# Performance work log

Measured on AMD Instinct MI355X. Metric: run time of the kernel, lower is better.

## Reference

```python
import jax, jax.numpy as jnp
import numpy as np

B, S, D = 1, 2048, 4096
N_HEADS, N_KV_HEADS = 32, 8
HEAD_DIM = D // N_HEADS  # 128


def setup_inputs() -> dict:
    key = jax.random.key(0)
    ks = jax.random.split(key, 6)
    x = jax.random.normal(ks[0], (B, S, D), dtype=jnp.float32)
    # weights stored as [in, out] so forward is x @ W (== torch x @ W.T with W [out,in])
    sc = 0.02
    wq = jax.random.normal(ks[1], (D, N_HEADS * HEAD_DIM), dtype=jnp.float32) * sc
    wk = jax.random.normal(ks[2], (D, N_KV_HEADS * HEAD_DIM), dtype=jnp.float32) * sc
    wv = jax.random.normal(ks[3], (D, N_KV_HEADS * HEAD_DIM), dtype=jnp.float32) * sc
    wo = jax.random.normal(ks[4], (N_HEADS * HEAD_DIM, D), dtype=jnp.float32) * sc
    # rotary tables: freqs_cis as cos/sin of shape [S, HEAD_DIM//2]
    inv_freq = 1.0 / (10000.0 ** (np.arange(0, HEAD_DIM, 2, dtype=np.float32) / HEAD_DIM))
    t = np.arange(S, dtype=np.float32)
    freqs = np.outer(t, inv_freq)  # [S, HEAD_DIM//2]
    cos = jnp.asarray(np.cos(freqs), dtype=jnp.float32)
    sin = jnp.asarray(np.sin(freqs), dtype=jnp.float32)
    # additive causal mask [S, S]: 0 on/below diagonal, -inf above
    mask = jnp.where(jnp.tril(jnp.ones((S, S), dtype=bool)), 0.0, -1e9).astype(jnp.float32)
    return {"x": x, "wq": wq, "wk": wk, "wv": wv, "wo": wo,
            "cos": cos, "sin": sin, "mask": mask}


def _apply_rope(t, cos, sin):
    # t: [B, S, H, Hd]; interpret last dim as Hd//2 complex pairs (interleaved)
    b, s, h, hd = t.shape
    tr = t.reshape(b, s, h, hd // 2, 2)
    t1, t2 = tr[..., 0], tr[..., 1]
    c = cos[None, :, None, :]  # [1, S, 1, Hd//2]
    sn = sin[None, :, None, :]
    o1 = t1 * c - t2 * sn
    o2 = t1 * sn + t2 * c
    return jnp.stack([o1, o2], axis=-1).reshape(b, s, h, hd)


def reference(x, wq, wk, wv, wo, cos, sin, mask):
    b, s, d = x.shape
    hd = 2 * cos.shape[-1]
    nh = wq.shape[1] // hd
    nkv = wk.shape[1] // hd
    n_rep = nh // nkv
    q = (x @ wq).reshape(b, s, nh, hd)
    k = (x @ wk).reshape(b, s, nkv, hd)
    v = (x @ wv).reshape(b, s, nkv, hd)
    q = _apply_rope(q, cos, sin)
    k = _apply_rope(k, cos, sin)
    # repeat_kv along head dim
    k = jnp.repeat(k, n_rep, axis=2)  # [B, S, H, Hd]
    v = jnp.repeat(v, n_rep, axis=2)
    scale = 1.0 / jnp.sqrt(jnp.float32(hd))
    scores = jnp.einsum('bqhd,bkhd->bhqk', q, k) * scale + mask[None, None, :, :]
    probs = jax.nn.softmax(scores, axis=-1)
    out = jnp.einsum('bhqk,bkhd->bqhd', probs, v).reshape(b, s, nh * hd)
    return out @ wo
```

## Files before the change

kernel.cpp:

```cpp
#include <hip/hip_runtime.h>
#include <hip/hip_bf16.h>

typedef unsigned short u16;
typedef unsigned int   u32;
typedef __attribute__((ext_vector_type(8))) short bf16x8;
typedef __attribute__((ext_vector_type(4))) short bf16x4;
typedef __attribute__((ext_vector_type(4))) float f32x4;
typedef __attribute__((ext_vector_type(4))) unsigned short u16x4;

__device__ __forceinline__ u16 f32_to_bf16bits(float f) {
    u32 x = __float_as_uint(f);
    u32 r = (x + 0x7fffu + ((x >> 16) & 1u)) >> 16;
    return (u16)r;
}
__device__ __forceinline__ float bf16bits_to_f32(u16 u) {
    return __uint_as_float(((u32)u) << 16);
}
__device__ __forceinline__ u32 cvt_pk_bf16(float lo, float hi) {
    u32 r;
    asm("v_cvt_pk_bf16_f32 %0, %1, %2" : "=v"(r) : "v"(lo), "v"(hi));
    return r;
}

__device__ __forceinline__ void async_copy16(void* lds, const void* g) {
    __builtin_amdgcn_global_load_lds(
        (__attribute__((address_space(1))) void*)(g),
        (__attribute__((address_space(3))) void*)(lds), 16, 0, 0);
}

__global__ void convert_f32_bf16(const float* __restrict__ src, u16* __restrict__ dst, int n4) {
    const int i = blockIdx.x * 256 + threadIdx.x;
    if (i >= n4) return;
    const float4 v = ((const float4*)src)[i];
    u16x4 o = { f32_to_bf16bits(v.x), f32_to_bf16bits(v.y),
                f32_to_bf16bits(v.z), f32_to_bf16bits(v.w) };
    ((u16x4*)dst)[i] = o;
}

__global__ void transpose_wT(const float* __restrict__ src, u16* __restrict__ dst,
                             int N, int dstStride) {
    __shared__ float tile[32][129];
    const int n0 = blockIdx.x * 128, k0 = blockIdx.y * 32;
    const int tx = threadIdx.x, ty = threadIdx.y;
#pragma unroll
    for (int j = 0; j < 4; ++j)
#pragma unroll
        for (int i = 0; i < 4; ++i)
            tile[ty + 8*j][tx + 32*i] = src[(size_t)(k0 + ty + 8*j) * N + n0 + tx + 32*i];
    __syncthreads();
    const int tid = ty * 32 + tx;
    const int c = tid & 15, nl0 = tid >> 4;
#pragma unroll
    for (int s = 0; s < 8; ++s) {
        const int nl = nl0 + s * 16;
        const u32 pk = (u32)f32_to_bf16bits(tile[2*c][nl])
                     | ((u32)f32_to_bf16bits(tile[2*c + 1][nl]) << 16);
        *(u32*)&dst[(size_t)(n0 + nl) * dstStride + k0 + 2*c] = pk;
    }
}

__global__ void transpose_v(const u16* __restrict__ qkv, u16* __restrict__ vT) {
    __shared__ u16 tile[32][34];
    const int s0 = blockIdx.x * 32, n0 = blockIdx.y * 32;
    const int tx = threadIdx.x, ty = threadIdx.y;
#pragma unroll
    for (int i = 0; i < 4; ++i)
        tile[ty + i*8][tx] = qkv[(size_t)(s0 + ty + i*8) * 6144 + 5120 + n0 + tx];
    __syncthreads();
#pragma unroll
    for (int i = 0; i < 4; ++i)
        vT[(size_t)(n0 + ty + i*8) * 2048 + s0 + tx] = tile[tx][ty + i*8];
}

__global__ void rope_kernel(u32* __restrict__ qkv, const float* __restrict__ cosp,
                            const float* __restrict__ sinp) {
    const int s = blockIdx.x;
    const int h = blockIdx.y * 4 + (threadIdx.x >> 6);
    const int p = threadIdx.x & 63;
    const size_t off = ((size_t)s * 6144 + h * 128) >> 1;
    const u32 packed = qkv[off + p];
    const float c  = cosp[s*64 + p], sn = sinp[s*64 + p];
    const float t1 = bf16bits_to_f32((u16)(packed & 0xffffu));
    const float t2 = bf16bits_to_f32((u16)(packed >> 16));
    const float o1 = t1 * c - t2 * sn;
    const float o2 = t1 * sn + t2 * c;
    qkv[off + p] = (u32)f32_to_bf16bits(o1) | ((u32)f32_to_bf16bits(o2) << 16);
}

template<int MFRAG, bool BF16OUT>
__global__ __launch_bounds__(512, 2) void gemm_ring(
    const u16* __restrict__ A, const u16* __restrict__ B, void* __restrict__ Cv,
    int N, int K, int nbn) {
    constexpr int BM     = MFRAG * 32;
    constexpr int ABYTES = BM * 64;
    constexpr int SLOT   = ABYTES + 16384;
    __shared__ __align__(16) char sm[4 * SLOT];

    const int tid = threadIdx.x;
    const int w = tid >> 6, l = tid & 63;
    const int wm = w >> 2, wn = w & 3;
    const int g = l >> 4, c0 = l & 15;
    const int bid = blockIdx.x;
    const int bm = bid / nbn, bn = bid % nbn;

    const int srow   = l >> 2;
    const int schunk = (l & 3) ^ (srow & 3) ^ ((srow >> 2) & 3);
    const u16* As = A + (size_t)(bm * BM  + w*16 + srow) * K + schunk * 8;
    const u16* Bs = B + (size_t)(bn * 256 + w*16 + srow) * K + schunk * 8;

    const int rswz = ((g ^ (c0 & 3) ^ ((c0 >> 2) & 3)) & 3) * 16;

    f32x4 acc[MFRAG][4] = {};

    auto stage = [&](int st, int ss) {
        char* aB = sm + ss * SLOT;
        char* bB = aB + ABYTES;
        const u16* as = As + (size_t)st * 32;
        const u16* bs = Bs + (size_t)st * 32;
        async_copy16(aB + (w*16) * 64, as);
        if (MFRAG == 8)
            async_copy16(aB + (128 + w*16) * 64, as + (size_t)128 * K);
        async_copy16(bB + (w*16) * 64, bs);
        async_copy16(bB + (128 + w*16) * 64, bs + (size_t)128 * K);
    };

    const int nkt = K >> 5;
    stage(0, 0);
    stage(1, 1);

    for (int kt = 0; kt < nkt; ++kt) {
        const int st = (kt + 2 < nkt) ? kt + 2 : nkt - 1;
        stage(st, (kt + 2) & 3);
        if (MFRAG == 8) asm volatile("s_waitcnt vmcnt(8)" ::: "memory");
        else            asm volatile("s_waitcnt vmcnt(6)" ::: "memory");
        __builtin_amdgcn_s_barrier();
        asm volatile("" ::: "memory");

        const char* aB = sm + (kt & 3) * SLOT;
        const char* bB = aB + ABYTES;
        bf16x8 bfr[4];
#pragma unroll
        for (int n = 0; n < 4; ++n)
            bfr[n] = *(const bf16x8*)(bB + (wn*64 + n*16 + c0) * 64 + rswz);
        bf16x8 afr[MFRAG];
#pragma unroll
        for (int m = 0; m < MFRAG; ++m)
            afr[m] = *(const bf16x8*)(aB + (wm*(BM/2) + m*16 + c0) * 64 + rswz);

        __builtin_amdgcn_s_setprio(1);
#pragma unroll
        for (int m = 0; m < MFRAG; ++m)
#pragma unroll
            for (int n = 0; n < 4; ++n)
                acc[m][n] = __builtin_amdgcn_mfma_f32_16x16x32_bf16(
                    afr[m], bfr[n], acc[m][n], 0, 0, 0);
        __builtin_amdgcn_s_setprio(0);
        asm volatile("" ::: "memory");
    }
    asm volatile("s_waitcnt vmcnt(0)" ::: "memory");

#pragma unroll
    for (int m = 0; m < MFRAG; ++m)
#pragma unroll
        for (int n = 0; n < 4; ++n) {
            const int row = bm*BM + wm*(BM/2) + m*16 + g*4;
            const int col = bn*256 + wn*64 + n*16 + c0;
#pragma unroll
            for (int r = 0; r < 4; ++r) {
                if (BF16OUT)
                    ((u16*)Cv)[(size_t)(row + r) * N + col] = f32_to_bf16bits(acc[m][n][r]);
                else
                    ((float*)Cv)[(size_t)(row + r) * N + col] = acc[m][n][r];
            }
        }
}

__global__ __launch_bounds__(256, 2) void attn_kernel(
    const u16* __restrict__ qkv, const u16* __restrict__ vT, u16* __restrict__ outp) {
    __shared__ __align__(16) char lds[65536];
    const int tid = threadIdx.x;
    const int w = tid >> 6, l = tid & 63;
    const int g = l >> 4, c0 = l & 15;
    const int qt = (blockIdx.y < 16) ? blockIdx.x : (15 - (int)blockIdx.x);
    const int h = blockIdx.y;
    const int kvh = h >> 2;
    const int q0g = qt * 128;
    const int qrow0 = q0g + w * 32;

    const int srK = w*4 + g,        scK = c0 ^ srK;
    const int srV = w*8 + (l >> 3), scV = (l & 7) ^ (l >> 3);

#pragma unroll
    for (int i = 0; i < 8; ++i)
        async_copy16(lds + (i*16 + w*4) * 256,
                     qkv + (size_t)(q0g + i*16 + srK) * 6144 + h*128 + scK*8);
    __syncthreads();

#pragma unroll
    for (int i = 0; i < 4; ++i)
        async_copy16(lds + 32768 + (i*16 + w*4) * 256,
                     qkv + (size_t)(i*16 + srK) * 6144 + 4096 + kvh*128 + scK*8);
#pragma unroll
    for (int i = 0; i < 4; ++i)
        async_copy16(lds + 49152 + (i*32 + w*8) * 128,
                     vT + (size_t)(kvh*128 + i*32 + srV) * 2048 + scV*8);

    bf16x8 qf[2][4];
#pragma unroll
    for (int i = 0; i < 2; ++i)
#pragma unroll
        for (int dks = 0; dks < 4; ++dks) {
            const int row = w*32 + i*16 + c0;
            qf[i][dks] = *(const bf16x8*)(lds + row*256 + (((dks*4 + g) ^ c0) * 16));
        }
    __syncthreads();

    f32x4 o[2][8] = {};
    float lsum[2] = {0.f, 0.f};
    const int ntiles = 2*qt + 2;
    const float SC2 = 0.08838834764831845f * 1.4426950408889634f;

    for (int kt = 0; kt < ntiles; ++kt) {
        const int cur = kt & 1;
        const char* kb = lds + (cur ? 0 : 32768);
        const char* vb = lds + (cur ? 16384 : 49152);
        if (kt + 1 < ntiles) {
            char* kbn = lds + ((cur ^ 1) ? 0 : 32768);
            char* vbn = lds + ((cur ^ 1) ? 16384 : 49152);
#pragma unroll
            for (int i = 0; i < 4; ++i)
                async_copy16(kbn + (i*16 + w*4) * 256,
                             qkv + (size_t)((kt+1)*64 + i*16 + srK) * 6144 + 4096 + kvh*128 + scK*8);
#pragma unroll
            for (int i = 0; i < 4; ++i)
                async_copy16(vbn + (i*32 + w*8) * 128,
                             vT + (size_t)(kvh*128 + i*32 + srV) * 2048 + (kt+1)*64 + scV*8);
        }

        if (kt*64 <= qrow0 + 31) {
            f32x4 st[2][4] = {};
            __builtin_amdgcn_s_setprio(1);
#pragma unroll
            for (int dks = 0; dks < 4; ++dks) {
                bf16x8 kf[4];
#pragma unroll
                for (int j = 0; j < 4; ++j) {
                    const int row = j*16 + c0;
                    kf[j] = *(const bf16x8*)(kb + row*256 + (((dks*4 + g) ^ c0) * 16));
                }
#pragma unroll
                for (int i = 0; i < 2; ++i)
#pragma unroll
                    for (int j = 0; j < 4; ++j)
                        st[i][j] = __builtin_amdgcn_mfma_f32_16x16x32_bf16(
                            kf[j], qf[i][dks], st[i][j], 0, 0, 0);
            }
            __builtin_amdgcn_s_setprio(0);

            const bool diag = (kt*64 + 63) > qrow0;
            u32 pk[2][4][2];
#pragma unroll
            for (int i = 0; i < 2; ++i) {
                float rowsum = 0.f;
#pragma unroll
                for (int j = 0; j < 4; ++j) {
#pragma unroll
                    for (int r = 0; r < 4; ++r) {
                        float p = exp2f(st[i][j][r] * SC2);
                        if (diag) {
                            const int kgl = kt*64 + j*16 + g*4 + r;
                            const int qgl = qrow0 + i*16 + c0;
                            if (kgl > qgl) p = 0.f;
                        }
                        st[i][j][r] = p;
                        rowsum += p;
                    }
                    pk[i][j][0] = cvt_pk_bf16(st[i][j][0], st[i][j][1]);
                    pk[i][j][1] = cvt_pk_bf16(st[i][j][2], st[i][j][3]);
                }
                rowsum += __shfl_xor(rowsum, 16);
                rowsum += __shfl_xor(rowsum, 32);
                lsum[i] += rowsum;
            }

#pragma unroll
            for (int dks = 0; dks < 2; ++dks) {
                bf16x8 pf[2];
#pragma unroll
                for (int i = 0; i < 2; ++i) {
                    union { u32 u[4]; bf16x8 v; } pu;
                    pu.u[0] = pk[i][2*dks][0];   pu.u[1] = pk[i][2*dks][1];
                    pu.u[2] = pk[i][2*dks+1][0]; pu.u[3] = pk[i][2*dks+1][1];
                    pf[i] = pu.v;
                }
                __builtin_amdgcn_s_setprio(1);
#pragma unroll
                for (int dj = 0; dj < 8; ++dj) {
                    const int row = dj*16 + c0;
                    const int cg0 = (4*dks + (g >> 1)) ^ (row & 7);
                    const int cg1 = (4*dks + (g >> 1) + 2) ^ (row & 7);
                    union { struct { bf16x4 lo, hi; } p; bf16x8 v; } vu;
                    vu.p.lo = *(const bf16x4*)(vb + row*128 + cg0*16 + 8*(g & 1));
                    vu.p.hi = *(const bf16x4*)(vb + row*128 + cg1*16 + 8*(g & 1));
#pragma unroll
                    for (int i = 0; i < 2; ++i)
                        o[i][dj] = __builtin_amdgcn_mfma_f32_16x16x32_bf16(
                            vu.v, pf[i], o[i][dj], 0, 0, 0);
                }
                __builtin_amdgcn_s_setprio(0);
            }
        }
        __syncthreads();
    }

#pragma unroll
    for (int i = 0; i < 2; ++i) {
        const float rcp = 1.0f / lsum[i];
        const int qg = qrow0 + i*16 + c0;
#pragma unroll
        for (int dj = 0; dj < 8; ++dj) {
            u16x4 ov = { f32_to_bf16bits(o[i][dj][0] * rcp),
                         f32_to_bf16bits(o[i][dj][1] * rcp),
                         f32_to_bf16bits(o[i][dj][2] * rcp),
                         f32_to_bf16bits(o[i][dj][3] * rcp) };
            *(u16x4*)(outp + (size_t)qg * 4096 + h*128 + dj*16 + g*4) = ov;
        }
    }
}

extern "C" void kernel_launch(void* const* d_in, const int* in_sizes, int n_in,
                              void* d_out, int out_size, void* d_ws, size_t ws_size,
                              hipStream_t stream) {
    const float* x    = (const float*)d_in[0];
    const float* wq   = (const float*)d_in[1];
    const float* wk   = (const float*)d_in[2];
    const float* wv   = (const float*)d_in[3];
    const float* wo   = (const float*)d_in[4];
    const float* cosp = (const float*)d_in[5];
    const float* sinp = (const float*)d_in[6];

    char* ws = (char*)d_ws;
    u16* xb    = (u16*)(ws);
    u16* wqkvT = (u16*)(ws + 16777216);
    u16* woT   = (u16*)(ws + 67108864);
    u16* qkv   = (u16*)(ws + 100663296);
    u16* vTb   = (u16*)(ws + 125829120);
    u16* attn  = (u16*)(ws + 130023424);

    dim3 tb(32, 8);
    convert_f32_bf16<<<8192, 256, 0, stream>>>(x, xb, 2097152);
    transpose_wT<<<dim3(32, 128), tb, 0, stream>>>(wq, wqkvT, 4096, 4096);
    transpose_wT<<<dim3(8, 128),  tb, 0, stream>>>(wk, wqkvT + (size_t)4096*4096, 1024, 4096);
    transpose_wT<<<dim3(8, 128),  tb, 0, stream>>>(wv, wqkvT + (size_t)5120*4096, 1024, 4096);
    transpose_wT<<<dim3(32, 128), tb, 0, stream>>>(wo, woT, 4096, 4096);

    gemm_ring<8, true><<<192, 512, 0, stream>>>(xb, wqkvT, qkv, 6144, 4096, 24);
    rope_kernel<<<dim3(2048, 10), 256, 0, stream>>>((u32*)qkv, cosp, sinp);
    transpose_v<<<dim3(64, 32), tb, 0, stream>>>(qkv, vTb);
    attn_kernel<<<dim3(16, 32), 256, 0, stream>>>(qkv, vTb, attn);
    gemm_ring<4, false><<<256, 512, 0, stream>>>(attn, woT, d_out, 4096, 4096, 16);
}
```

Baseline: 330.3 us.

## Replace ring GEMM with 8-phase ping-pong pipelined GEMM using K=64 tiles

```diff
diff --git a/kernel.cpp b/kernel.cpp
--- a/kernel.cpp
+++ b/kernel.cpp
@@ -87,80 +87,108 @@
     qkv[off + p] = (u32)f32_to_bf16bits(o1) | ((u32)f32_to_bf16bits(o2) << 16);
 }
 
-template<int MFRAG, bool BF16OUT>
-__global__ __launch_bounds__(512, 2) void gemm_ring(
+#define RD_A(d, mh) do { _Pragma("unroll")                                    \
+    for (int mi = 0; mi < MREP/2; ++mi) {                                     \
+        const char* ab = sm + ((d)*2 + wm)*HALF_A                             \
+                       + (((mh)*(MREP/2)+mi)*16 + c0)*128;                    \
+        af[mi][0] = *(const bf16x8*)(ab + ((g ^ (c0&7)) * 16));               \
+        af[mi][1] = *(const bf16x8*)(ab + (((4+g) ^ (c0&7)) * 16));           \
+    } } while (0)
+
+#define RD_B(d, nh) do { _Pragma("unroll")                                    \
+    for (int ni = 0; ni < 2; ++ni) {                                          \
+        const char* bb = sm + BOFF + ((d)*2 + bh)*16384                       \
+                       + ((wn&1)*64 + ((nh)*2+ni)*16 + c0)*128;               \
+        bf[(nh)*2+ni][0] = *(const bf16x8*)(bb + ((g ^ (c0&7)) * 16));        \
+        bf[(nh)*2+ni][1] = *(const bf16x8*)(bb + (((4+g) ^ (c0&7)) * 16));    \
+    } } while (0)
+
+#define MFMA_PH(mh, nh) do {                                                  \
+    __builtin_amdgcn_s_barrier();                                             \
+    asm volatile("s_waitcnt lgkmcnt(0)" ::: "memory");                        \
+    __builtin_amdgcn_sched_barrier(0);                                        \
+    __builtin_amdgcn_s_setprio(1);                                            \
+    _Pragma("unroll") for (int dk = 0; dk < 2; ++dk)                          \
+    _Pragma("unroll") for (int mi = 0; mi < MREP/2; ++mi)                     \
+    _Pragma("unroll") for (int ni = 0; ni < 2; ++ni)                          \
+        acc[(mh)*(MREP/2)+mi][(nh)*2+ni] =                                    \
+            __builtin_amdgcn_mfma_f32_16x16x32_bf16(                          \
+                af[mi][dk], bf[(nh)*2+ni][dk],                                \
+                acc[(mh)*(MREP/2)+mi][(nh)*2+ni], 0, 0, 0);                   \
+    __builtin_amdgcn_s_setprio(0); } while (0)
+
+#define ENDBAR() __builtin_amdgcn_s_barrier()
+#define VMC4()   asm volatile("s_waitcnt vmcnt(4)" ::: "memory")
+
+template<int MREP, bool BF16OUT>
+__global__ __launch_bounds__(512, 2) void gemm8p(
     const u16* __restrict__ A, const u16* __restrict__ B, void* __restrict__ Cv,
-    int N, int K, int nbn) {
-    constexpr int BM     = MFRAG * 32;
-    constexpr int ABYTES = BM * 64;
-    constexpr int SLOT   = ABYTES + 16384;
-    __shared__ __align__(16) char sm[4 * SLOT];
+    const int N, const int K, const int nbn) {
+    constexpr int BM     = MREP * 32;
+    constexpr int HALF_A = (BM/2) * 128;
+    constexpr int BOFF   = 4 * HALF_A;
+    __shared__ __align__(16) char sm[BOFF + 65536];
 
     const int tid = threadIdx.x;
     const int w = tid >> 6, l = tid & 63;
-    const int wm = w >> 2, wn = w & 3;
+    const int wm = w >> 2, wn = w & 3, bh = wn >> 1;
     const int g = l >> 4, c0 = l & 15;
-    const int bid = blockIdx.x;
-    const int bm = bid / nbn, bn = bid % nbn;
-
-    const int srow   = l >> 2;
-    const int schunk = (l & 3) ^ (srow & 3) ^ ((srow >> 2) & 3);
-    const u16* As = A + (size_t)(bm * BM  + w*16 + srow) * K + schunk * 8;
-    const u16* Bs = B + (size_t)(bn * 256 + w*16 + srow) * K + schunk * 8;
-
-    const int rswz = ((g ^ (c0 & 3) ^ ((c0 >> 2) & 3)) & 3) * 16;
-
-    f32x4 acc[MFRAG][4] = {};
-
-    auto stage = [&](int st, int ss) {
-        char* aB = sm + ss * SLOT;
-        char* bB = aB + ABYTES;
-        const u16* as = As + (size_t)st * 32;
-        const u16* bs = Bs + (size_t)st * 32;
-        async_copy16(aB + (w*16) * 64, as);
-        if (MFRAG == 8)
-            async_copy16(aB + (128 + w*16) * 64, as + (size_t)128 * K);
-        async_copy16(bB + (w*16) * 64, bs);
-        async_copy16(bB + (128 + w*16) * 64, bs + (size_t)128 * K);
+    const int bm = blockIdx.x / nbn, bn = blockIdx.x % nbn;
+
+    const int srow   = w*8 + (l >> 3);
+    const int schunk = (l & 7) ^ (l >> 3);
+    const u16* Abase = A + (size_t)(bm*BM  + srow) * K + schunk*8;
+    const u16* Bbase = B + (size_t)(bn*256 + srow) * K + schunk*8;
+
+    f32x4 acc[MREP][4] = {};
+    bf16x8 af[MREP/2][2], bf[4][2];
+
+    auto stageA = [&](int kt, int d, int h) {
+        char* dst = sm + (d*2 + h) * HALF_A + (w*8) * 128;
+        const u16* src = Abase + (size_t)h*(BM/2)*K + kt*64;
+#pragma unroll
+        for (int r = 0; r < MREP/4; ++r)
+            async_copy16(dst + r*64*128, src + (size_t)r*64*K);
     };
-
-    const int nkt = K >> 5;
-    stage(0, 0);
-    stage(1, 1);
-
-    for (int kt = 0; kt < nkt; ++kt) {
-        const int st = (kt + 2 < nkt) ? kt + 2 : nkt - 1;
-        stage(st, (kt + 2) & 3);
-        if (MFRAG == 8) asm volatile("s_waitcnt vmcnt(8)" ::: "memory");
-        else            asm volatile("s_waitcnt vmcnt(6)" ::: "memory");
-        __builtin_amdgcn_s_barrier();
-        asm volatile("" ::: "memory");
-
-        const char* aB = sm + (kt & 3) * SLOT;
-        const char* bB = aB + ABYTES;
-        bf16x8 bfr[4];
-#pragma unroll
-        for (int n = 0; n < 4; ++n)
-            bfr[n] = *(const bf16x8*)(bB + (wn*64 + n*16 + c0) * 64 + rswz);
-        bf16x8 afr[MFRAG];
-#pragma unroll
-        for (int m = 0; m < MFRAG; ++m)
-            afr[m] = *(const bf16x8*)(aB + (wm*(BM/2) + m*16 + c0) * 64 + rswz);
-
-        __builtin_amdgcn_s_setprio(1);
-#pragma unroll
-        for (int m = 0; m < MFRAG; ++m)
-#pragma unroll
-            for (int n = 0; n < 4; ++n)
-                acc[m][n] = __builtin_amdgcn_mfma_f32_16x16x32_bf16(
-                    afr[m], bfr[n], acc[m][n], 0, 0, 0);
-        __builtin_amdgcn_s_setprio(0);
-        asm volatile("" ::: "memory");
+    auto stageB = [&](int kt, int d, int h) {
+        char* dst = sm + BOFF + (d*2 + h) * 16384 + (w*8) * 128;
+        const u16* src = Bbase + (size_t)h*128*K + kt*64;
+#pragma unroll
+        for (int r = 0; r < 2; ++r)
+            async_copy16(dst + r*64*128, src + (size_t)r*64*K);
+    };
+
+    const int nkt = K >> 6;
+
+    stageB(0, 0, 0); stageB(0, 0, 1);
+    stageA(0, 0, 0); stageA(0, 0, 1);
+    stageB(1, 1, 0); stageB(1, 1, 1);
+    VMC4();
+    __builtin_amdgcn_s_barrier();
+
+    for (int t = 0; t < nkt; t += 2) {
+        const int tb = t + 1, tc = t + 2, td = t + 3;
+        RD_A(0, 0); RD_B(0, 0); stageA(tb, 1, 0);
+        MFMA_PH(0, 0); ENDBAR();
+        RD_B(0, 1); stageA(tb, 1, 1);
+        MFMA_PH(0, 1); ENDBAR();
+        RD_A(0, 1); if (tc < nkt) stageB(tc, 0, 0);
+        MFMA_PH(1, 0); ENDBAR();
+        if (tc < nkt) stageB(tc, 0, 1);
+        MFMA_PH(1, 1); VMC4(); ENDBAR();
+        RD_A(1, 0); RD_B(1, 0); if (tc < nkt) stageA(tc, 0, 0);
+        MFMA_PH(0, 0); ENDBAR();
+        RD_B(1, 1); if (tc < nkt) stageA(tc, 0, 1);
+        MFMA_PH(0, 1); ENDBAR();
+        RD_A(1, 1); if (td < nkt) stageB(td, 1, 0);
+        MFMA_PH(1, 0); ENDBAR();
+        if (td < nkt) stageB(td, 1, 1);
+        MFMA_PH(1, 1); VMC4(); ENDBAR();
     }
     asm volatile("s_waitcnt vmcnt(0)" ::: "memory");
 
 #pragma unroll
-    for (int m = 0; m < MFRAG; ++m)
+    for (int m = 0; m < MREP; ++m)
 #pragma unroll
         for (int n = 0; n < 4; ++n) {
             const int row = bm*BM + wm*(BM/2) + m*16 + g*4;
@@ -174,6 +202,11 @@
             }
         }
 }
+#undef RD_A
+#undef RD_B
+#undef MFMA_PH
+#undef ENDBAR
+#undef VMC4
 
 __global__ __launch_bounds__(256, 2) void attn_kernel(
     const u16* __restrict__ qkv, const u16* __restrict__ vT, u16* __restrict__ outp) {
@@ -354,9 +387,9 @@
     transpose_wT<<<dim3(8, 128),  tb, 0, stream>>>(wv, wqkvT + (size_t)5120*4096, 1024, 4096);
     transpose_wT<<<dim3(32, 128), tb, 0, stream>>>(wo, woT, 4096, 4096);
 
-    gemm_ring<8, true><<<192, 512, 0, stream>>>(xb, wqkvT, qkv, 6144, 4096, 24);
+    gemm8p<8, true><<<192, 512, 0, stream>>>(xb, wqkvT, qkv, 6144, 4096, 24);
     rope_kernel<<<dim3(2048, 10), 256, 0, stream>>>((u32*)qkv, cosp, sinp);
     transpose_v<<<dim3(64, 32), tb, 0, stream>>>(qkv, vTb);
     attn_kernel<<<dim3(16, 32), 256, 0, stream>>>(qkv, vTb, attn);
-    gemm_ring<4, false><<<256, 512, 0, stream>>>(attn, woT, d_out, 4096, 4096, 16);
-}
+    gemm8p<4, false><<<256, 512, 0, stream>>>(attn, woT, d_out, 4096, 4096, 16);
+}
```

New measurement: 315.4 us. 1.05x faster.

## Replace ring GEMM with split-phase pipelined QKV and output GEMMs using BK=64

Applied to the files above, without the earlier changes.

```diff
diff --git a/kernel.cpp b/kernel.cpp
--- a/kernel.cpp
+++ b/kernel.cpp
@@ -27,6 +27,10 @@
         (__attribute__((address_space(1))) void*)(g),
         (__attribute__((address_space(3))) void*)(lds), 16, 0, 0);
 }
+
+#define VMC6() asm volatile("s_waitcnt vmcnt(6)" ::: "memory")
+#define VMC0() asm volatile("s_waitcnt vmcnt(0)" ::: "memory")
+#define ENDBAR() __builtin_amdgcn_s_barrier()
 
 __global__ void convert_f32_bf16(const float* __restrict__ src, u16* __restrict__ dst, int n4) {
     const int i = blockIdx.x * 256 + threadIdx.x;
@@ -87,93 +91,202 @@
     qkv[off + p] = (u32)f32_to_bf16bits(o1) | ((u32)f32_to_bf16bits(o2) << 16);
 }
 
-template<int MFRAG, bool BF16OUT>
-__global__ __launch_bounds__(512, 2) void gemm_ring(
-    const u16* __restrict__ A, const u16* __restrict__ B, void* __restrict__ Cv,
-    int N, int K, int nbn) {
-    constexpr int BM     = MFRAG * 32;
-    constexpr int ABYTES = BM * 64;
-    constexpr int SLOT   = ABYTES + 16384;
-    __shared__ __align__(16) char sm[4 * SLOT];
-
+#define Q_RD_A(d, mh) do { _Pragma("unroll")                                   \
+    for (int mi = 0; mi < 2; ++mi) {                                           \
+        const char* ab = sm + ((d)*2 + wm)*8192 + (((mh)*2+mi)*16 + c0)*128;   \
+        af[mi][0] = *(const bf16x8*)(ab + ((g ^ (c0&7)) * 16));                \
+        af[mi][1] = *(const bf16x8*)(ab + (((4+g) ^ (c0&7)) * 16));            \
+    } } while (0)
+
+#define Q_RD_B(d, nh) do { _Pragma("unroll")                                   \
+    for (int ni = 0; ni < 3; ++ni) {                                           \
+        const char* bb = sm + 32768 + ((d)*2 + bh)*24576                       \
+                       + ((wn&1)*96 + ((nh)*3+ni)*16 + c0)*128;                \
+        bf[(nh)*3+ni][0] = *(const bf16x8*)(bb + ((g ^ (c0&7)) * 16));         \
+        bf[(nh)*3+ni][1] = *(const bf16x8*)(bb + (((4+g) ^ (c0&7)) * 16));     \
+    } } while (0)
+
+#define Q_MFMA(mh, nh) do {                                                    \
+    __builtin_amdgcn_s_barrier();                                              \
+    asm volatile("s_waitcnt lgkmcnt(0)" ::: "memory");                         \
+    __builtin_amdgcn_sched_barrier(0);                                         \
+    __builtin_amdgcn_s_setprio(1);                                             \
+    _Pragma("unroll") for (int dk = 0; dk < 2; ++dk)                           \
+    _Pragma("unroll") for (int mi = 0; mi < 2; ++mi)                           \
+    _Pragma("unroll") for (int ni = 0; ni < 3; ++ni)                           \
+        acc[(mh)*2+mi][(nh)*3+ni] = __builtin_amdgcn_mfma_f32_16x16x32_bf16(   \
+            af[mi][dk], bf[(nh)*3+ni][dk], acc[(mh)*2+mi][(nh)*3+ni], 0,0,0);  \
+    __builtin_amdgcn_s_setprio(0); } while (0)
+
+__global__ __launch_bounds__(512, 2) void gemm_qkv(
+    const u16* __restrict__ A, const u16* __restrict__ B, u16* __restrict__ C,
+    const int N, const int K) {
+    __shared__ __align__(16) char sm[131072];
+    const int tid = threadIdx.x;
+    const int w = tid >> 6, l = tid & 63;
+    const int wm = w >> 2, wn = w & 3, bh = wn >> 1;
+    const int g = l >> 4, c0 = l & 15;
+    const int bm = blockIdx.x >> 4, bn = blockIdx.x & 15;
+
+    const int srow   = w*8 + (l >> 3);
+    const int schunk = (l & 7) ^ (l >> 3);
+    const u16* Abase = A + (size_t)(bm*128 + srow) * K + schunk*8;
+    const u16* Bbase = B + (size_t)(bn*384 + srow) * K + schunk*8;
+
+    f32x4 acc[4][6] = {};
+    bf16x8 af[2][2], bf[6][2];
+
+    auto stageA = [&](int kt, int d, int h) {
+        async_copy16(sm + (d*2 + h)*8192 + (w*8)*128,
+                     Abase + (size_t)h*64*K + kt*64);
+    };
+    auto stageB = [&](int kt, int d, int h) {
+        char* dst = sm + 32768 + (d*2 + h)*24576 + (w*8)*128;
+        const u16* src = Bbase + (size_t)h*192*K + kt*64;
+#pragma unroll
+        for (int r = 0; r < 3; ++r)
+            async_copy16(dst + r*8192, src + (size_t)r*64*K);
+    };
+
+    const int nkt = K >> 6;
+
+    stageB(0, 0, 0); stageB(0, 0, 1);
+    stageA(0, 0, 0); stageA(0, 0, 1);
+    stageB(1, 1, 0); stageB(1, 1, 1);
+    VMC6();
+    __builtin_amdgcn_s_barrier();
+
+    for (int t = 0; t < nkt; t += 2) {
+        const int tb = t + 1, tc = t + 2, td = t + 3;
+        Q_RD_A(0, 0); Q_RD_B(0, 0); stageA(tb, 1, 0);
+        Q_MFMA(0, 0); ENDBAR();
+        Q_RD_B(0, 1); stageA(tb, 1, 1);
+        Q_MFMA(0, 1); ENDBAR();
+        Q_RD_A(0, 1); if (tc < nkt) stageB(tc, 0, 0);
+        Q_MFMA(1, 0); ENDBAR();
+        if (tc < nkt) { stageB(tc, 0, 1); Q_MFMA(1, 1); VMC6(); }
+        else          { Q_MFMA(1, 1); VMC0(); }
+        ENDBAR();
+        Q_RD_A(1, 0); Q_RD_B(1, 0); if (tc < nkt) stageA(tc, 0, 0);
+        Q_MFMA(0, 0); ENDBAR();
+        Q_RD_B(1, 1); if (tc < nkt) stageA(tc, 0, 1);
+        Q_MFMA(0, 1); ENDBAR();
+        Q_RD_A(1, 1); if (td < nkt) stageB(td, 1, 0);
+        Q_MFMA(1, 0); ENDBAR();
+        if (td < nkt) { stageB(td, 1, 1); Q_MFMA(1, 1); VMC6(); }
+        else          { Q_MFMA(1, 1); VMC0(); }
+        ENDBAR();
+    }
+    VMC0();
+
+#pragma unroll
+    for (int m = 0; m < 4; ++m)
+#pragma unroll
+        for (int n = 0; n < 6; ++n) {
+            const int row = bm*128 + wm*64 + m*16 + g*4;
+            const int col = bn*384 + wn*96 + n*16 + c0;
+#pragma unroll
+            for (int r = 0; r < 4; ++r)
+                C[(size_t)(row + r) * N + col] = f32_to_bf16bits(acc[m][n][r]);
+        }
+}
+#undef Q_RD_A
+#undef Q_RD_B
+#undef Q_MFMA
+
+#define O_RD_A(b, mh) do { _Pragma("unroll")                                   \
+    for (int mi = 0; mi < 2; ++mi) {                                           \
+        const char* ab = sm + (b)*49152 + (wm*64 + ((mh)*2+mi)*16 + c0)*128;   \
+        af[mi][0] = *(const bf16x8*)(ab + ((g ^ (c0&7)) * 16));                \
+        af[mi][1] = *(const bf16x8*)(ab + (((4+g) ^ (c0&7)) * 16));            \
+    } } while (0)
+
+#define O_RD_B(b) do { _Pragma("unroll")                                       \
+    for (int nj = 0; nj < 4; ++nj) {                                           \
+        const char* bb = sm + (b)*49152 + 16384 + (wn*64 + nj*16 + c0)*128;    \
+        bf[nj][0] = *(const bf16x8*)(bb + ((g ^ (c0&7)) * 16));                \
+        bf[nj][1] = *(const bf16x8*)(bb + (((4+g) ^ (c0&7)) * 16));            \
+    } } while (0)
+
+#define O_MFMA(mh) do {                                                        \
+    __builtin_amdgcn_s_barrier();                                              \
+    asm volatile("s_waitcnt lgkmcnt(0)" ::: "memory");                         \
+    __builtin_amdgcn_sched_barrier(0);                                         \
+    __builtin_amdgcn_s_setprio(1);                                             \
+    _Pragma("unroll") for (int dk = 0; dk < 2; ++dk)                           \
+    _Pragma("unroll") for (int mi = 0; mi < 2; ++mi)                           \
+    _Pragma("unroll") for (int nj = 0; nj < 4; ++nj)                           \
+        acc[(mh)*2+mi][nj] = __builtin_amdgcn_mfma_f32_16x16x32_bf16(          \
+            af[mi][dk], bf[nj][dk], acc[(mh)*2+mi][nj], 0,0,0);                \
+    __builtin_amdgcn_s_setprio(0); } while (0)
+
+__global__ __launch_bounds__(512, 2) void gemm_out(
+    const u16* __restrict__ A, const u16* __restrict__ B, float* __restrict__ C,
+    const int N, const int K) {
+    __shared__ __align__(16) char sm[147456];
     const int tid = threadIdx.x;
     const int w = tid >> 6, l = tid & 63;
     const int wm = w >> 2, wn = w & 3;
     const int g = l >> 4, c0 = l & 15;
-    const int bid = blockIdx.x;
-    const int bm = bid / nbn, bn = bid % nbn;
-
-    const int srow   = l >> 2;
-    const int schunk = (l & 3) ^ (srow & 3) ^ ((srow >> 2) & 3);
-    const u16* As = A + (size_t)(bm * BM  + w*16 + srow) * K + schunk * 8;
-    const u16* Bs = B + (size_t)(bn * 256 + w*16 + srow) * K + schunk * 8;
-
-    const int rswz = ((g ^ (c0 & 3) ^ ((c0 >> 2) & 3)) & 3) * 16;
-
-    f32x4 acc[MFRAG][4] = {};
-
-    auto stage = [&](int st, int ss) {
-        char* aB = sm + ss * SLOT;
-        char* bB = aB + ABYTES;
-        const u16* as = As + (size_t)st * 32;
-        const u16* bs = Bs + (size_t)st * 32;
-        async_copy16(aB + (w*16) * 64, as);
-        if (MFRAG == 8)
-            async_copy16(aB + (128 + w*16) * 64, as + (size_t)128 * K);
-        async_copy16(bB + (w*16) * 64, bs);
-        async_copy16(bB + (128 + w*16) * 64, bs + (size_t)128 * K);
+    const int bm = blockIdx.x >> 4, bn = blockIdx.x & 15;
+
+    const int srow   = w*8 + (l >> 3);
+    const int schunk = (l & 7) ^ (l >> 3);
+    const u16* Abase = A + (size_t)(bm*128 + srow) * K + schunk*8;
+    const u16* Bbase = B + (size_t)(bn*256 + srow) * K + schunk*8;
+
+    f32x4 acc[4][4] = {};
+    bf16x8 af[2][2], bf[4][2];
+
+    auto stage_p0 = [&](int kt, int b) {
+        char* base = sm + b*49152 + (w*8)*128;
+        async_copy16(base,                 Abase + kt*64);
+        async_copy16(base + 16384,         Bbase + kt*64);
+        async_copy16(base + 16384 + 8192,  Bbase + (size_t)64*K + kt*64);
     };
-
-    const int nkt = K >> 5;
-    stage(0, 0);
-    stage(1, 1);
-
-    for (int kt = 0; kt < nkt; ++kt) {
-        const int st = (kt + 2 < nkt) ? kt + 2 : nkt - 1;
-        stage(st, (kt + 2) & 3);
-        if (MFRAG == 8) asm volatile("s_waitcnt vmcnt(8)" ::: "memory");
-        else            asm volatile("s_waitcnt vmcnt(6)" ::: "memory");
-        __builtin_amdgcn_s_barrier();
-        asm volatile("" ::: "memory");
-
-        const char* aB = sm + (kt & 3) * SLOT;
-        const char* bB = aB + ABYTES;
-        bf16x8 bfr[4];
-#pragma unroll
-        for (int n = 0; n < 4; ++n)
-            bfr[n] = *(const bf16x8*)(bB + (wn*64 + n*16 + c0) * 64 + rswz);
-        bf16x8 afr[MFRAG];
-#pragma unroll
-        for (int m = 0; m < MFRAG; ++m)
-            afr[m] = *(const bf16x8*)(aB + (wm*(BM/2) + m*16 + c0) * 64 + rswz);
-
-        __builtin_amdgcn_s_setprio(1);
-#pragma unroll
-        for (int m = 0; m < MFRAG; ++m)
-#pragma unroll
-            for (int n = 0; n < 4; ++n)
-                acc[m][n] = __builtin_amdgcn_mfma_f32_16x16x32_bf16(
-                    afr[m], bfr[n], acc[m][n], 0, 0, 0);
-        __builtin_amdgcn_s_setprio(0);
-        asm volatile("" ::: "memory");
+    auto stage_p1 = [&](int kt, int b) {
+        char* base = sm + b*49152 + (w*8)*128;
+        async_copy16(base + 8192,          Abase + (size_t)64*K  + kt*64);
+        async_copy16(base + 16384 + 16384, Bbase + (size_t)128*K + kt*64);
+        async_copy16(base + 16384 + 24576, Bbase + (size_t)192*K + kt*64);
+    };
+
+    const int nkt = K >> 6;
+
+    stage_p0(0, 0); stage_p1(0, 0);
+    stage_p0(1, 1); stage_p1(1, 1);
+    VMC6();
+    __builtin_amdgcn_s_barrier();
+
+    int bc = 0;
+    for (int t = 0; t < nkt; ++t) {
+        const int b2 = (bc == 0) ? 2 : bc - 1;
+        const bool st = (t + 2) < nkt;
+        O_RD_A(bc, 0); O_RD_B(bc);
+        if (st) stage_p0(t + 2, b2);
+        O_MFMA(0); ENDBAR();
+        O_RD_A(bc, 1);
+        if (st) { stage_p1(t + 2, b2); O_MFMA(1); VMC6(); }
+        else    { O_MFMA(1); VMC0(); }
+        ENDBAR();
+        bc = (bc == 2) ? 0 : bc + 1;
     }
-    asm volatile("s_waitcnt vmcnt(0)" ::: "memory");
-
-#pragma unroll
-    for (int m = 0; m < MFRAG; ++m)
+    VMC0();
+
+#pragma unroll
+    for (int m = 0; m < 4; ++m)
 #pragma unroll
         for (int n = 0; n < 4; ++n) {
-            const int row = bm*BM + wm*(BM/2) + m*16 + g*4;
+            const int row = bm*128 + wm*64 + m*16 + g*4;
             const int col = bn*256 + wn*64 + n*16 + c0;
 #pragma unroll
-            for (int r = 0; r < 4; ++r) {
-                if (BF16OUT)
-                    ((u16*)Cv)[(size_t)(row + r) * N + col] = f32_to_bf16bits(acc[m][n][r]);
-                else
-                    ((float*)Cv)[(size_t)(row + r) * N + col] = acc[m][n][r];
-            }
-        }
-}
+            for (int r = 0; r < 4; ++r)
+                C[(size_t)(row + r) * N + col] = acc[m][n][r];
+        }
+}
+#undef O_RD_A
+#undef O_RD_B
+#undef O_MFMA
 
 __global__ __launch_bounds__(256, 2) void attn_kernel(
     const u16* __restrict__ qkv, const u16* __restrict__ vT, u16* __restrict__ outp) {
@@ -354,9 +467,9 @@
     transpose_wT<<<dim3(8, 128),  tb, 0, stream>>>(wv, wqkvT + (size_t)5120*4096, 1024, 4096);
     transpose_wT<<<dim3(32, 128), tb, 0, stream>>>(wo, woT, 4096, 4096);
 
-    gemm_ring<8, true><<<192, 512, 0, stream>>>(xb, wqkvT, qkv, 6144, 4096, 24);
+    gemm_qkv<<<256, 512, 0, stream>>>(xb, wqkvT, qkv, 6144, 4096);
     rope_kernel<<<dim3(2048, 10), 256, 0, stream>>>((u32*)qkv, cosp, sinp);
     transpose_v<<<dim3(64, 32), tb, 0, stream>>>(qkv, vTb);
     attn_kernel<<<dim3(16, 32), 256, 0, stream>>>(qkv, vTb, attn);
-    gemm_ring<4, false><<<256, 512, 0, stream>>>(attn, woT, d_out, 4096, 4096, 16);
-}
+    gemm_out<<<256, 512, 0, stream>>>(attn, woT, (float*)d_out, 4096, 4096);
+}
```

Result: faster. 317.6 us (-3.9%).

## Rewrite GEMMs with BK=64 double-buffered tiles and grid matching CU count

Applied to the files above, without the earlier changes.

```diff
diff --git a/kernel.cpp b/kernel.cpp
--- a/kernel.cpp
+++ b/kernel.cpp
@@ -27,6 +27,10 @@
         (__attribute__((address_space(1))) void*)(g),
         (__attribute__((address_space(3))) void*)(lds), 16, 0, 0);
 }
+
+#define VMCNT(n)  asm volatile("s_waitcnt vmcnt(" #n ")" ::: "memory")
+#define LGKMC0()  asm volatile("s_waitcnt lgkmcnt(0)" ::: "memory")
+#define ENDBAR()  __builtin_amdgcn_s_barrier()
 
 __global__ void convert_f32_bf16(const float* __restrict__ src, u16* __restrict__ dst, int n4) {
     const int i = blockIdx.x * 256 + threadIdx.x;
@@ -87,84 +91,94 @@
     qkv[off + p] = (u32)f32_to_bf16bits(o1) | ((u32)f32_to_bf16bits(o2) << 16);
 }
 
-template<int MFRAG, bool BF16OUT>
-__global__ __launch_bounds__(512, 2) void gemm_ring(
+template<int NF, bool BF16OUT>
+__global__ __launch_bounds__(512, 2) void gemm_big(
     const u16* __restrict__ A, const u16* __restrict__ B, void* __restrict__ Cv,
-    int N, int K, int nbn) {
-    constexpr int BM     = MFRAG * 32;
-    constexpr int ABYTES = BM * 64;
-    constexpr int SLOT   = ABYTES + 16384;
-    __shared__ __align__(16) char sm[4 * SLOT];
+    const int N, const int K) {
+    constexpr int BN     = NF * 64;
+    constexpr int BHALF  = (BN / 2) * 128;
+    constexpr int BCALLS = BHALF / 8192;
+    __shared__ __align__(16) char sm[32768 + 4 * BHALF];
 
     const int tid = threadIdx.x;
     const int w = tid >> 6, l = tid & 63;
-    const int wm = w >> 2, wn = w & 3;
+    const int wm = w >> 2, wn = w & 3, bh = wn >> 1;
     const int g = l >> 4, c0 = l & 15;
-    const int bid = blockIdx.x;
-    const int bm = bid / nbn, bn = bid % nbn;
-
-    const int srow   = l >> 2;
-    const int schunk = (l & 3) ^ (srow & 3) ^ ((srow >> 2) & 3);
-    const u16* As = A + (size_t)(bm * BM  + w*16 + srow) * K + schunk * 8;
-    const u16* Bs = B + (size_t)(bn * 256 + w*16 + srow) * K + schunk * 8;
-
-    const int rswz = ((g ^ (c0 & 3) ^ ((c0 >> 2) & 3)) & 3) * 16;
-
-    f32x4 acc[MFRAG][4] = {};
-
-    auto stage = [&](int st, int ss) {
-        char* aB = sm + ss * SLOT;
-        char* bB = aB + ABYTES;
-        const u16* as = As + (size_t)st * 32;
-        const u16* bs = Bs + (size_t)st * 32;
-        async_copy16(aB + (w*16) * 64, as);
-        if (MFRAG == 8)
-            async_copy16(aB + (128 + w*16) * 64, as + (size_t)128 * K);
-        async_copy16(bB + (w*16) * 64, bs);
-        async_copy16(bB + (128 + w*16) * 64, bs + (size_t)128 * K);
+    const int bm = blockIdx.x >> 4, bn = blockIdx.x & 15;
+
+    const int srow   = w*8 + (l >> 3);
+    const int schunk = (l & 7) ^ (l >> 3);
+    const u16* Abase = A + (size_t)(bm*128 + srow) * K + schunk*8;
+    const u16* Bbase = B + (size_t)(bn*BN  + srow) * K + schunk*8;
+
+    f32x4 acc[4][NF] = {};
+
+    auto stage = [&](int kt, int b) {
+#pragma unroll
+        for (int h = 0; h < 2; ++h)
+            async_copy16(sm + (b*2 + h)*8192 + (w*8)*128,
+                         Abase + (size_t)h*64*K + kt*64);
+#pragma unroll
+        for (int h = 0; h < 2; ++h) {
+            char* dst = sm + 32768 + (b*2 + h)*BHALF + (w*8)*128;
+            const u16* src = Bbase + (size_t)h*(BN/2)*K + kt*64;
+#pragma unroll
+            for (int r = 0; r < BCALLS; ++r)
+                async_copy16(dst + r*8192, src + (size_t)r*64*K);
+        }
     };
 
-    const int nkt = K >> 5;
+    const int nkt = K >> 6;
+
     stage(0, 0);
     stage(1, 1);
-
-    for (int kt = 0; kt < nkt; ++kt) {
-        const int st = (kt + 2 < nkt) ? kt + 2 : nkt - 1;
-        stage(st, (kt + 2) & 3);
-        if (MFRAG == 8) asm volatile("s_waitcnt vmcnt(8)" ::: "memory");
-        else            asm volatile("s_waitcnt vmcnt(6)" ::: "memory");
-        __builtin_amdgcn_s_barrier();
-        asm volatile("" ::: "memory");
-
-        const char* aB = sm + (kt & 3) * SLOT;
-        const char* bB = aB + ABYTES;
-        bf16x8 bfr[4];
-#pragma unroll
-        for (int n = 0; n < 4; ++n)
-            bfr[n] = *(const bf16x8*)(bB + (wn*64 + n*16 + c0) * 64 + rswz);
-        bf16x8 afr[MFRAG];
-#pragma unroll
-        for (int m = 0; m < MFRAG; ++m)
-            afr[m] = *(const bf16x8*)(aB + (wm*(BM/2) + m*16 + c0) * 64 + rswz);
-
+    if constexpr (NF == 6) VMCNT(8); else VMCNT(6);
+    ENDBAR();
+
+    for (int t = 0; t < nkt; ++t) {
+        const int b = t & 1;
+        bf16x8 afr[4][2], bfr[NF][2];
+#pragma unroll
+        for (int dk = 0; dk < 2; ++dk) {
+#pragma unroll
+            for (int mi = 0; mi < 4; ++mi) {
+                const char* ab = sm + (b*2 + wm)*8192 + (mi*16 + c0)*128;
+                afr[mi][dk] = *(const bf16x8*)(ab + (((dk*4 + g) ^ (c0 & 7)) * 16));
+            }
+#pragma unroll
+            for (int ni = 0; ni < NF; ++ni) {
+                const char* bb = sm + 32768 + (b*2 + bh)*BHALF
+                               + ((wn & 1)*(BN/4) + ni*16 + c0)*128;
+                bfr[ni][dk] = *(const bf16x8*)(bb + (((dk*4 + g) ^ (c0 & 7)) * 16));
+            }
+        }
         __builtin_amdgcn_s_setprio(1);
 #pragma unroll
-        for (int m = 0; m < MFRAG; ++m)
-#pragma unroll
-            for (int n = 0; n < 4; ++n)
-                acc[m][n] = __builtin_amdgcn_mfma_f32_16x16x32_bf16(
-                    afr[m], bfr[n], acc[m][n], 0, 0, 0);
+        for (int dk = 0; dk < 2; ++dk)
+#pragma unroll
+            for (int mi = 0; mi < 4; ++mi)
+#pragma unroll
+                for (int ni = 0; ni < NF; ++ni)
+                    acc[mi][ni] = __builtin_amdgcn_mfma_f32_16x16x32_bf16(
+                        afr[mi][dk], bfr[ni][dk], acc[mi][ni], 0, 0, 0);
         __builtin_amdgcn_s_setprio(0);
-        asm volatile("" ::: "memory");
+        LGKMC0();
+        ENDBAR();
+        if (t + 2 < nkt) {
+            stage(t + 2, b);
+            if constexpr (NF == 6) VMCNT(8); else VMCNT(6);
+        } else {
+            VMCNT(0);
+        }
+        ENDBAR();
     }
-    asm volatile("s_waitcnt vmcnt(0)" ::: "memory");
-
-#pragma unroll
-    for (int m = 0; m < MFRAG; ++m)
-#pragma unroll
-        for (int n = 0; n < 4; ++n) {
-            const int row = bm*BM + wm*(BM/2) + m*16 + g*4;
-            const int col = bn*256 + wn*64 + n*16 + c0;
+
+#pragma unroll
+    for (int m = 0; m < 4; ++m)
+#pragma unroll
+        for (int n = 0; n < NF; ++n) {
+            const int row = bm*128 + wm*64 + m*16 + g*4;
+            const int col = bn*BN + wn*(BN/4) + n*16 + c0;
 #pragma unroll
             for (int r = 0; r < 4; ++r) {
                 if (BF16OUT)
@@ -354,9 +368,9 @@
     transpose_wT<<<dim3(8, 128),  tb, 0, stream>>>(wv, wqkvT + (size_t)5120*4096, 1024, 4096);
     transpose_wT<<<dim3(32, 128), tb, 0, stream>>>(wo, woT, 4096, 4096);
 
-    gemm_ring<8, true><<<192, 512, 0, stream>>>(xb, wqkvT, qkv, 6144, 4096, 24);
+    gemm_big<6, true><<<256, 512, 0, stream>>>(xb, wqkvT, qkv, 6144, 4096);
     rope_kernel<<<dim3(2048, 10), 256, 0, stream>>>((u32*)qkv, cosp, sinp);
     transpose_v<<<dim3(64, 32), tb, 0, stream>>>(qkv, vTb);
     attn_kernel<<<dim3(16, 32), 256, 0, stream>>>(qkv, vTb, attn);
-    gemm_ring<4, false><<<256, 512, 0, stream>>>(attn, woT, d_out, 4096, 4096, 16);
-}
+    gemm_big<4, false><<<256, 512, 0, stream>>>(attn, woT, d_out, 4096, 4096);
+}
```

Measured after the change: 324.7 us. No clear change (-1.7%).
